# Kernel optimization log

Hardware: AMD Instinct MI355X
Metric: run time of the kernel (lower is better)

Reference implementation:

```python
import jax, jax.numpy as jnp
import numpy as np

BETA = 0.25


def setup_inputs() -> dict:
    key = jax.random.key(0)
    k1, k2 = jax.random.split(key)
    N, K, D = 65536, 1024, 256
    z = jax.random.normal(k1, (N, D), dtype=jnp.float32)
    # EmbeddingEMA initializes weight uniform in [-1, 1]
    weight = jax.random.uniform(k2, (K, D), dtype=jnp.float32, minval=-1.0, maxval=1.0)
    return {"z": z, "weight": weight}


def reference(z, weight):
    # z: [N, D] flattened latents; weight: [K, D] codebook
    z_flat = z.reshape(-1, weight.shape[1])
    # squared euclidean distances via ||z||^2 + ||e||^2 - 2 z e^T
    d = (
        jnp.sum(z_flat * z_flat, axis=1, keepdims=True)
        + jnp.sum(weight * weight, axis=1)
        - 2.0 * jnp.matmul(z_flat, weight.T)
    )  # [N, K]
    min_encoding_indices = jnp.argmin(d, axis=1)  # [N]
    z_q = weight[min_encoding_indices].reshape(z.shape)  # embedding lookup
    # commitment loss: beta * mse(stop_grad(z_q), z)
    loss = BETA * jnp.mean((jax.lax.stop_gradient(z_q) - z) ** 2)
    # straight-through estimator
    z_q_st = z + jax.lax.stop_gradient(z_q - z)
    return (loss, z_q_st, min_encoding_indices)
```

## Files before the change

### kernel.cpp

```cpp
#include <hip/hip_runtime.h>
#include <hip/hip_bf16.h>

typedef float f32x4 __attribute__((ext_vector_type(4)));
typedef short short8 __attribute__((ext_vector_type(8)));

#define NTOT   65536
#define DDIM   256
#define KCODES 1024
#define BRR    128
#define CT     64
#define IDXOFF 16777217
#define MARGIN_T4 0.015f


__device__ __forceinline__ unsigned short bf16_rne(float x) {
  unsigned u = __float_as_uint(x);
  return (unsigned short)((u + 0x7fff + ((u >> 16) & 1)) >> 16);
}

__global__ __launch_bounds__(256) void wsq_kernel(const float* __restrict__ w,
                                                  float* __restrict__ wsq) {
  int k = blockIdx.x * 256 + threadIdx.x;
  if (k >= KCODES) return;
  const f32x4* wr = (const f32x4*)(w + (size_t)k * DDIM);
  float s = 0.f;
#pragma unroll 8
  for (int j = 0; j < DDIM / 4; ++j) {
    f32x4 v = wr[j];
    s += v[0] * v[0] + v[1] * v[1] + v[2] * v[2] + v[3] * v[3];
  }
  wsq[k] = s;
}

__global__ __launch_bounds__(256) void prep_w(const float* __restrict__ w,
                                              float* __restrict__ wplanes) {
  int t = blockIdx.x * 256 + threadIdx.x;
  int k = t >> 6;
  int d = (t & 63) * 4;
  f32x4 v = *(const f32x4*)(w + (size_t)k * DDIM + d);
  unsigned h[4], l[4];
#pragma unroll
  for (int j = 0; j < 4; ++j) {
    unsigned short hb = bf16_rne(v[j]);
    float hf = __uint_as_float(((unsigned)hb) << 16);
    h[j] = hb;
    l[j] = bf16_rne(v[j] - hf);
  }
  int ct = k >> 6, row = k & 63, dc = d >> 6, dloc = d & 63;
  size_t base = (size_t)(ct * 4 + dc) * 16384;
  int off = row * 128 + ((dloc * 2) ^ ((row & 7) << 4));
  *(int2*)((char*)wplanes + base + off) =
      make_int2((int)(h[0] | (h[1] << 16)), (int)(h[2] | (h[3] << 16)));
  *(int2*)((char*)wplanes + base + 8192 + off) =
      make_int2((int)(l[0] | (l[1] << 16)), (int)(l[2] | (l[3] << 16)));
}

__device__ __forceinline__ void stage_tile_z(const float* __restrict__ gsrc,
                                             short* hi_t, short* lo_t, int tid) {
#pragma unroll
  for (int it = 0; it < 8; ++it) {
    int flat4 = it * 256 + tid;
    int row = flat4 >> 4;
    int c4 = (flat4 & 15) * 4;
    f32x4 v = *(const f32x4*)(gsrc + (size_t)row * DDIM + c4);
    unsigned h[4], l[4];
#pragma unroll
    for (int j = 0; j < 4; ++j) {
      unsigned short hb = bf16_rne(v[j]);
      float hf = __uint_as_float(((unsigned)hb) << 16);
      h[j] = hb;
      l[j] = bf16_rne(v[j] - hf);
    }
    int off = row * 128 + ((c4 * 2) ^ ((row & 7) << 4));
    *(int2*)((char*)hi_t + off) = make_int2((int)(h[0] | (h[1] << 16)), (int)(h[2] | (h[3] << 16)));
    *(int2*)((char*)lo_t + off) = make_int2((int)(l[0] | (l[1] << 16)), (int)(l[2] | (l[3] << 16)));
  }
}

__device__ __forceinline__ void stage_w2(const float* __restrict__ wpl, int pr,
                                         char* buf, int tid) {
  const char* g = (const char*)wpl + (size_t)pr * 32768 + tid * 16;
  char* l = buf + ((tid >> 6) << 10);
#pragma unroll
  for (int i = 0; i < 8; ++i)
    __builtin_amdgcn_global_load_lds(
        (const __attribute__((address_space(1))) unsigned int*)(g + i * 4096),
        (__attribute__((address_space(3))) unsigned int*)(l + i * 4096), 16, 0, 0);
}

#define INS4(S0, S1, S2, S3, I0, I1, I2, I3, os, oi)                        \
  if (os < S3 || (os == S3 && oi < I3)) {                                   \
    if (os < S2 || (os == S2 && oi < I2)) {                                 \
      S3 = S2; I3 = I2;                                                     \
      if (os < S1 || (os == S1 && oi < I1)) {                               \
        S2 = S1; I2 = I1;                                                   \
        if (os < S0 || (os == S0 && oi < I0)) {                             \
          S1 = S0; I1 = I0; S0 = os; I0 = oi;                               \
        } else { S1 = os; I1 = oi; }                                        \
      } else { S2 = os; I2 = oi; }                                          \
    } else { S3 = os; I3 = oi; }                                            \
  }

#define MFMA_STEP(DC, TB)                                                   \
  {                                                                         \
    _Pragma("unroll")                                                       \
    for (int ks = 0; ks < 2; ++ks) {                                        \
      _Pragma("unroll")                                                     \
      for (int mi = 0; mi < 4; ++mi) {                                      \
        const int row = mi * 16 + l15;                                      \
        const int off = row * 128 + (((ks * 64) + (lg * 16)) ^ ((row & 7) << 4)); \
        short8 ah = *(const short8*)((TB) + off);                           \
        short8 al = *(const short8*)((TB) + 8192 + off);                    \
        acc[mi][0] = __builtin_amdgcn_mfma_f32_16x16x32_bf16(ah, zf[DC][ks][0][0], acc[mi][0], 0, 0, 0); \
        acc[mi][0] = __builtin_amdgcn_mfma_f32_16x16x32_bf16(ah, zf[DC][ks][0][1], acc[mi][0], 0, 0, 0); \
        acc[mi][0] = __builtin_amdgcn_mfma_f32_16x16x32_bf16(al, zf[DC][ks][0][0], acc[mi][0], 0, 0, 0); \
        acc[mi][1] = __builtin_amdgcn_mfma_f32_16x16x32_bf16(ah, zf[DC][ks][1][0], acc[mi][1], 0, 0, 0); \
        acc[mi][1] = __builtin_amdgcn_mfma_f32_16x16x32_bf16(ah, zf[DC][ks][1][1], acc[mi][1], 0, 0, 0); \
        acc[mi][1] = __builtin_amdgcn_mfma_f32_16x16x32_bf16(al, zf[DC][ks][1][0], acc[mi][1], 0, 0, 0); \
      }                                                                     \
    }                                                                       \
  }

__global__ __launch_bounds__(256, 2) void vq_main(
    const float* __restrict__ z, const float* __restrict__ wplanes,
    const float* __restrict__ wsq, int* __restrict__ cand,
    int* __restrict__ flags, int* __restrict__ cnt, int* __restrict__ list) {
  __shared__ __align__(16) char lds[69632];
  char* buf0 = lds;
  char* buf1 = lds + 32768;
  float* wsq_l = (float*)(lds + 65536);

  const int tid = threadIdx.x;
  const int lane = tid & 63, wid = tid >> 6;
  const int l15 = lane & 15, lg = lane >> 4;
  const int br = blockIdx.x * BRR;

  for (int i = tid; i < KCODES; i += 256) wsq_l[i] = wsq[i];

  short8 zf[4][2][2][2];
  {
    short* zhi = (short*)lds;
    short* zlo = (short*)(lds + 16384);
    const int row0 = wid * 32 + l15, row1 = row0 + 16;
#pragma unroll
    for (int dc = 0; dc < 4; ++dc) {
      __syncthreads();
      stage_tile_z(z + (size_t)br * DDIM + dc * 64, zhi, zlo, tid);
      __syncthreads();
#pragma unroll
      for (int ks = 0; ks < 2; ++ks) {
        const int kb2 = (ks * 32 + lg * 8) * 2;
        const int off0 = row0 * 128 + (kb2 ^ ((row0 & 7) << 4));
        const int off1 = row1 * 128 + (kb2 ^ ((row1 & 7) << 4));
        zf[dc][ks][0][0] = *(const short8*)((char*)zhi + off0);
        zf[dc][ks][0][1] = *(const short8*)((char*)zlo + off0);
        zf[dc][ks][1][0] = *(const short8*)((char*)zhi + off1);
        zf[dc][ks][1][1] = *(const short8*)((char*)zlo + off1);
      }
    }
    __syncthreads();
  }

  float a0 = 3.4e38f, a1 = 3.4e38f, a2 = 3.4e38f, a3 = 3.4e38f;
  int e0 = 0x7fffffff, e1 = 0x7fffffff, e2 = 0x7fffffff, e3 = 0x7fffffff;
  float c0 = 3.4e38f, c1 = 3.4e38f, c2 = 3.4e38f, c3 = 3.4e38f;
  int f0 = 0x7fffffff, f1 = 0x7fffffff, f2 = 0x7fffffff, f3 = 0x7fffffff;

  stage_w2(wplanes, 0, buf0, tid);
  __syncthreads();

  for (int ct = 0; ct < 16; ++ct) {
    f32x4 acc[4][2];
#pragma unroll
    for (int mi = 0; mi < 4; ++mi)
#pragma unroll
      for (int ni = 0; ni < 2; ++ni) acc[mi][ni] = (f32x4){0.f, 0.f, 0.f, 0.f};

    stage_w2(wplanes, ct * 2 + 1, buf1, tid);
    MFMA_STEP(0, buf0)
    MFMA_STEP(1, buf0 + 16384)
    __syncthreads();
    if (ct < 15) stage_w2(wplanes, ct * 2 + 2, buf0, tid);
    MFMA_STEP(2, buf1)
    MFMA_STEP(3, buf1 + 16384)
    __syncthreads();

    const int kb = ct * CT;
#pragma unroll
    for (int mi = 0; mi < 4; ++mi)
#pragma unroll
      for (int rg = 0; rg < 4; ++rg) {
        const int cg = kb + mi * 16 + lg * 4 + rg;
        const float w2 = wsq_l[cg];
        float s0v = fmaf(-2.f, acc[mi][0][rg], w2);
        if (s0v < a3 || (s0v == a3 && cg < e3)) { INS4(a0, a1, a2, a3, e0, e1, e2, e3, s0v, cg); }
        float s1v = fmaf(-2.f, acc[mi][1][rg], w2);
        if (s1v < c3 || (s1v == c3 && cg < f3)) { INS4(c0, c1, c2, c3, f0, f1, f2, f3, s1v, cg); }
      }
  }

#pragma unroll
  for (int m = 16; m <= 32; m <<= 1) {
    float os[4]; int oi[4];
    os[0] = __shfl_xor(a0, m); oi[0] = __shfl_xor(e0, m);
    os[1] = __shfl_xor(a1, m); oi[1] = __shfl_xor(e1, m);
    os[2] = __shfl_xor(a2, m); oi[2] = __shfl_xor(e2, m);
    os[3] = __shfl_xor(a3, m); oi[3] = __shfl_xor(e3, m);
#pragma unroll
    for (int t = 0; t < 4; ++t) { INS4(a0, a1, a2, a3, e0, e1, e2, e3, os[t], oi[t]); }
    os[0] = __shfl_xor(c0, m); oi[0] = __shfl_xor(f0, m);
    os[1] = __shfl_xor(c1, m); oi[1] = __shfl_xor(f1, m);
    os[2] = __shfl_xor(c2, m); oi[2] = __shfl_xor(f2, m);
    os[3] = __shfl_xor(c3, m); oi[3] = __shfl_xor(f3, m);
#pragma unroll
    for (int t = 0; t < 4; ++t) { INS4(c0, c1, c2, c3, f0, f1, f2, f3, os[t], oi[t]); }
  }

  if (lg == 0) {
    {
      int grow = br + wid * 32 + l15;
      *(int4*)&cand[(size_t)grow * 4] = make_int4(e0, e1, e2, e3);
      int flg = (a3 - a0 < MARGIN_T4) ? 1 : 0;
      flags[grow] = flg;
      if (flg) { int p = atomicAdd(cnt, 1); list[p] = grow; }
    }
    {
      int grow = br + wid * 32 + 16 + l15;
      *(int4*)&cand[(size_t)grow * 4] = make_int4(f0, f1, f2, f3);
      int flg = (c3 - c0 < MARGIN_T4) ? 1 : 0;
      flags[grow] = flg;
      if (flg) { int p = atomicAdd(cnt, 1); list[p] = grow; }
    }
  }
}

__global__ __launch_bounds__(256) void refine_fused(
    const float* __restrict__ z, const float* __restrict__ w,
    const float* __restrict__ wsq, const int* __restrict__ cand,
    const int* __restrict__ flags, float* __restrict__ buckets,
    float* __restrict__ out) {
  __shared__ float ws4[4];
  const int tid = threadIdx.x, lane = tid & 63, wv = tid >> 6;
  float lsum = 0.f;
  for (int r = blockIdx.x * 4 + wv; r < NTOT; r += gridDim.x * 4) {
    if (flags[r]) continue;
    const int4 c4 = *(const int4*)&cand[(size_t)r * 4];
    f32x4 zv = *(const f32x4*)(z + (size_t)r * DDIM + lane * 4);
    f32x4 w0 = *(const f32x4*)(w + (size_t)c4.x * DDIM + lane * 4);
    f32x4 w1 = *(const f32x4*)(w + (size_t)c4.y * DDIM + lane * 4);
    f32x4 w2 = *(const f32x4*)(w + (size_t)c4.z * DDIM + lane * 4);
    f32x4 w3 = *(const f32x4*)(w + (size_t)c4.w * DDIM + lane * 4);
    float p0 = fmaf(zv[0], w0[0], fmaf(zv[1], w0[1], fmaf(zv[2], w0[2], zv[3] * w0[3])));
    float p1 = fmaf(zv[0], w1[0], fmaf(zv[1], w1[1], fmaf(zv[2], w1[2], zv[3] * w1[3])));
    float p2 = fmaf(zv[0], w2[0], fmaf(zv[1], w2[1], fmaf(zv[2], w2[2], zv[3] * w2[3])));
    float p3 = fmaf(zv[0], w3[0], fmaf(zv[1], w3[1], fmaf(zv[2], w3[2], zv[3] * w3[3])));
#pragma unroll
    for (int m = 1; m <= 32; m <<= 1) {
      p0 += __shfl_xor(p0, m);
      p1 += __shfl_xor(p1, m);
      p2 += __shfl_xor(p2, m);
      p3 += __shfl_xor(p3, m);
    }
    float s0 = fmaf(-2.f, p0, wsq[c4.x]);
    float s1 = fmaf(-2.f, p1, wsq[c4.y]);
    float s2 = fmaf(-2.f, p2, wsq[c4.z]);
    float s3 = fmaf(-2.f, p3, wsq[c4.w]);
    float bs = s0; int bi = c4.x;
    if (s1 < bs || (s1 == bs && c4.y < bi)) { bs = s1; bi = c4.y; }
    if (s2 < bs || (s2 == bs && c4.z < bi)) { bs = s2; bi = c4.z; }
    if (s3 < bs || (s3 == bs && c4.w < bi)) { bs = s3; bi = c4.w; }
    f32x4 qv = *(const f32x4*)(w + (size_t)bi * DDIM + lane * 4);
    f32x4 o;
#pragma unroll
    for (int j = 0; j < 4; ++j) {
      float df = qv[j] - zv[j];
      o[j] = zv[j] + df;
      lsum = fmaf(df, df, lsum);
    }
    *(f32x4*)(out + 1 + (size_t)r * DDIM + lane * 4) = o;
    if (lane == 0) out[(size_t)IDXOFF + r] = (float)bi;
  }
#pragma unroll
  for (int m = 1; m <= 32; m <<= 1) lsum += __shfl_xor(lsum, m);
  if (lane == 0) ws4[wv] = lsum;
  __syncthreads();
  if (tid == 0)
    atomicAdd(&buckets[blockIdx.x & 63], ws4[0] + ws4[1] + ws4[2] + ws4[3]);
}

__global__ __launch_bounds__(256) void vq_refine(
    const float* __restrict__ z, const float* __restrict__ w,
    const float* __restrict__ wsq, float* __restrict__ buckets,
    const int* __restrict__ cnt, const int* __restrict__ list,
    float* __restrict__ out) {
  __shared__ __align__(16) float zrow[DDIM];
  __shared__ float rv[256];
  __shared__ int ri[256];
  const int tid = threadIdx.x;
  const int n = *cnt;
  for (int li = blockIdx.x; li < n; li += gridDim.x) {
    const int row = list[li];
    __syncthreads();
    zrow[tid] = z[(size_t)row * DDIM + tid];
    __syncthreads();
    float bv = 3.4e38f; int bi = 0;
#pragma unroll
    for (int c0 = 0; c0 < 4; ++c0) {
      int c = tid * 4 + c0;
      const f32x4* wr4 = (const f32x4*)(w + (size_t)c * DDIM);
      const f32x4* zr4 = (const f32x4*)zrow;
      f32x4 dv = {0.f, 0.f, 0.f, 0.f};
      for (int q = 0; q < DDIM / 4; ++q) {
        f32x4 a = zr4[q], b = wr4[q];
        dv[0] = fmaf(a[0], b[0], dv[0]); dv[1] = fmaf(a[1], b[1], dv[1]);
        dv[2] = fmaf(a[2], b[2], dv[2]); dv[3] = fmaf(a[3], b[3], dv[3]);
      }
      float s = fmaf(-2.f, (dv[0] + dv[1]) + (dv[2] + dv[3]), wsq[c]);
      if (s < bv) { bv = s; bi = c; }
    }
    rv[tid] = bv; ri[tid] = bi;
    __syncthreads();
    for (int s = 128; s > 0; s >>= 1) {
      if (tid < s) {
        float v2 = rv[tid + s]; int i2 = ri[tid + s];
        if (v2 < rv[tid] || (v2 == rv[tid] && i2 < ri[tid])) { rv[tid] = v2; ri[tid] = i2; }
      }
      __syncthreads();
    }
    const int idx = ri[0];
    if (tid == 0) out[(size_t)IDXOFF + row] = (float)idx;
    float qv = w[(size_t)idx * DDIM + tid];
    float zv = zrow[tid];
    float df = qv - zv;
    out[1 + (size_t)row * DDIM + tid] = zv + df;
    __syncthreads();
    rv[tid] = df * df;
    __syncthreads();
    for (int s = 128; s > 0; s >>= 1) {
      if (tid < s) rv[tid] += rv[tid + s];
      __syncthreads();
    }
    if (tid == 0) atomicAdd(&buckets[0], rv[0]);
  }
}

__global__ void vq_finalize(const float* __restrict__ buckets,
                            float* __restrict__ out) {
  float s = 0.f;
  for (int i = 0; i < 64; ++i) s += buckets[i];
  out[0] = 0.25f * s * (1.0f / 16777216.0f);
}

extern "C" void kernel_launch(void* const* d_in, const int* in_sizes, int n_in,
                              void* d_out, int out_size, void* d_ws, size_t ws_size,
                              hipStream_t stream) {
  const float* z = (const float*)d_in[0];
  const float* w = (const float*)d_in[1];
  float* out = (float*)d_out;
  float* wsf = (float*)d_ws;
  float* buckets = wsf;
  int* cnt = (int*)wsf + 64;
  float* wsq = wsf + 80;
  float* wplanes = wsf + 2048;
  int* cand = (int*)(wsf + 264192);
  int* flags = (int*)(wsf + 526336);
  int* list = (int*)(wsf + 591872);

  hipMemsetAsync(d_ws, 0, 320, stream);
  wsq_kernel<<<dim3(KCODES / 256), dim3(256), 0, stream>>>(w, wsq);
  prep_w<<<dim3(256), dim3(256), 0, stream>>>(w, wplanes);
  vq_main<<<dim3(NTOT / BRR), dim3(256), 0, stream>>>(z, wplanes, wsq, cand, flags, cnt, list);
  refine_fused<<<dim3(4096), dim3(256), 0, stream>>>(z, w, wsq, cand, flags, buckets, out);
  vq_refine<<<dim3(128), dim3(256), 0, stream>>>(z, w, wsq, buckets, cnt, list, out);
  vq_finalize<<<dim3(1), dim3(1), 0, stream>>>(buckets, out);
}
```

Measured before the change: 309.3 us.

## Fuse gather and loss into main VQ kernel, track top-2 with margin patch

Replaces the per-row top-4 candidate list and the separate candidate rescoring kernel with a top-2 margin check inside the main kernel. The main kernel now writes indices, gathers z_q, writes the output and accumulates the loss directly, so the cand/flags buffers and one launch disappear. Rows with a small top-2 gap are queued to a patch kernel that recomputes them exactly in fp32 and corrects the loss by a delta. The weight staging is split into smaller single-plane double-buffered chunks, which halves LDS use. The cost is more syncs per tile and a wider margin (0.04), which may queue more rows for the exact fp32 fallback.

```diff
diff --git a/kernel.cpp b/kernel.cpp
--- a/kernel.cpp
+++ b/kernel.cpp
@@ -10,7 +10,7 @@
 #define BRR    128
 #define CT     64
 #define IDXOFF 16777217
-#define MARGIN_T4 0.015f
+#define MARGIN 0.04f
 
 
 __device__ __forceinline__ unsigned short bf16_rne(float x) {
@@ -77,29 +77,16 @@
   }
 }
 
-__device__ __forceinline__ void stage_w2(const float* __restrict__ wpl, int pr,
-                                         char* buf, int tid) {
-  const char* g = (const char*)wpl + (size_t)pr * 32768 + tid * 16;
+__device__ __forceinline__ void stage_w(const float* __restrict__ wpl, int st,
+                                        char* buf, int tid) {
+  const char* g = (const char*)wpl + (size_t)st * 16384 + tid * 16;
   char* l = buf + ((tid >> 6) << 10);
 #pragma unroll
-  for (int i = 0; i < 8; ++i)
+  for (int i = 0; i < 4; ++i)
     __builtin_amdgcn_global_load_lds(
         (const __attribute__((address_space(1))) unsigned int*)(g + i * 4096),
         (__attribute__((address_space(3))) unsigned int*)(l + i * 4096), 16, 0, 0);
 }
-
-#define INS4(S0, S1, S2, S3, I0, I1, I2, I3, os, oi)                        \
-  if (os < S3 || (os == S3 && oi < I3)) {                                   \
-    if (os < S2 || (os == S2 && oi < I2)) {                                 \
-      S3 = S2; I3 = I2;                                                     \
-      if (os < S1 || (os == S1 && oi < I1)) {                               \
-        S2 = S1; I2 = I1;                                                   \
-        if (os < S0 || (os == S0 && oi < I0)) {                             \
-          S1 = S0; I1 = I0; S0 = os; I0 = oi;                               \
-        } else { S1 = os; I1 = oi; }                                        \
-      } else { S2 = os; I2 = oi; }                                          \
-    } else { S3 = os; I3 = oi; }                                            \
-  }
 
 #define MFMA_STEP(DC, TB)                                                   \
   {                                                                         \
@@ -122,13 +109,16 @@
   }
 
 __global__ __launch_bounds__(256, 2) void vq_main(
-    const float* __restrict__ z, const float* __restrict__ wplanes,
-    const float* __restrict__ wsq, int* __restrict__ cand,
-    int* __restrict__ flags, int* __restrict__ cnt, int* __restrict__ list) {
-  __shared__ __align__(16) char lds[69632];
+    const float* __restrict__ z, const float* __restrict__ w,
+    const float* __restrict__ wplanes, const float* __restrict__ wsq,
+    float* __restrict__ buckets, int* __restrict__ cnt, int* __restrict__ list,
+    float* __restrict__ out) {
+  __shared__ __align__(16) char lds[36864];
   char* buf0 = lds;
-  char* buf1 = lds + 32768;
-  float* wsq_l = (float*)(lds + 65536);
+  char* buf1 = lds + 16384;
+  float* wsq_l = (float*)(lds + 32768);
+  __shared__ int sidx[BRR];
+  __shared__ float ws4[4];
 
   const int tid = threadIdx.x;
   const int lane = tid & 63, wid = tid >> 6;
@@ -161,12 +151,10 @@
     __syncthreads();
   }
 
-  float a0 = 3.4e38f, a1 = 3.4e38f, a2 = 3.4e38f, a3 = 3.4e38f;
-  int e0 = 0x7fffffff, e1 = 0x7fffffff, e2 = 0x7fffffff, e3 = 0x7fffffff;
-  float c0 = 3.4e38f, c1 = 3.4e38f, c2 = 3.4e38f, c3 = 3.4e38f;
-  int f0 = 0x7fffffff, f1 = 0x7fffffff, f2 = 0x7fffffff, f3 = 0x7fffffff;
-
-  stage_w2(wplanes, 0, buf0, tid);
+  float m1[2] = {3.4e38f, 3.4e38f}, m2[2] = {3.4e38f, 3.4e38f};
+  int i1[2] = {0x7fffffff, 0x7fffffff};
+
+  stage_w(wplanes, 0, buf0, tid);
   __syncthreads();
 
   for (int ct = 0; ct < 16; ++ct) {
@@ -176,119 +164,75 @@
 #pragma unroll
       for (int ni = 0; ni < 2; ++ni) acc[mi][ni] = (f32x4){0.f, 0.f, 0.f, 0.f};
 
-    stage_w2(wplanes, ct * 2 + 1, buf1, tid);
-    MFMA_STEP(0, buf0)
-    MFMA_STEP(1, buf0 + 16384)
-    __syncthreads();
-    if (ct < 15) stage_w2(wplanes, ct * 2 + 2, buf0, tid);
-    MFMA_STEP(2, buf1)
-    MFMA_STEP(3, buf1 + 16384)
-    __syncthreads();
+#pragma unroll
+    for (int dc = 0; dc < 4; ++dc) {
+      const int st = ct * 4 + dc;
+      char* cbuf = (st & 1) ? buf1 : buf0;
+      char* nbuf = (st & 1) ? buf0 : buf1;
+      if (st < 63) stage_w(wplanes, st + 1, nbuf, tid);
+      MFMA_STEP(dc, cbuf)
+      __syncthreads();
+    }
 
     const int kb = ct * CT;
 #pragma unroll
-    for (int mi = 0; mi < 4; ++mi)
-#pragma unroll
-      for (int rg = 0; rg < 4; ++rg) {
-        const int cg = kb + mi * 16 + lg * 4 + rg;
-        const float w2 = wsq_l[cg];
-        float s0v = fmaf(-2.f, acc[mi][0][rg], w2);
-        if (s0v < a3 || (s0v == a3 && cg < e3)) { INS4(a0, a1, a2, a3, e0, e1, e2, e3, s0v, cg); }
-        float s1v = fmaf(-2.f, acc[mi][1][rg], w2);
-        if (s1v < c3 || (s1v == c3 && cg < f3)) { INS4(c0, c1, c2, c3, f0, f1, f2, f3, s1v, cg); }
+    for (int ni = 0; ni < 2; ++ni)
+#pragma unroll
+      for (int mi = 0; mi < 4; ++mi)
+#pragma unroll
+        for (int rg = 0; rg < 4; ++rg) {
+          const int cg = kb + mi * 16 + lg * 4 + rg;
+          float s = fmaf(-2.f, acc[mi][ni][rg], wsq_l[cg]);
+          if (s < m1[ni]) { m2[ni] = m1[ni]; m1[ni] = s; i1[ni] = cg; }
+          else if (s < m2[ni]) m2[ni] = s;
+        }
+  }
+
+#pragma unroll
+  for (int ni = 0; ni < 2; ++ni) {
+#pragma unroll
+    for (int m = 16; m <= 32; m <<= 1) {
+      float om1 = __shfl_xor(m1[ni], m);
+      float om2 = __shfl_xor(m2[ni], m);
+      int oi1 = __shfl_xor(i1[ni], m);
+      if (om1 < m1[ni] || (om1 == m1[ni] && oi1 < i1[ni])) {
+        m2[ni] = fminf(m1[ni], om2); m1[ni] = om1; i1[ni] = oi1;
+      } else {
+        m2[ni] = fminf(m2[ni], om1);
       }
-  }
-
-#pragma unroll
-  for (int m = 16; m <= 32; m <<= 1) {
-    float os[4]; int oi[4];
-    os[0] = __shfl_xor(a0, m); oi[0] = __shfl_xor(e0, m);
-    os[1] = __shfl_xor(a1, m); oi[1] = __shfl_xor(e1, m);
-    os[2] = __shfl_xor(a2, m); oi[2] = __shfl_xor(e2, m);
-    os[3] = __shfl_xor(a3, m); oi[3] = __shfl_xor(e3, m);
-#pragma unroll
-    for (int t = 0; t < 4; ++t) { INS4(a0, a1, a2, a3, e0, e1, e2, e3, os[t], oi[t]); }
-    os[0] = __shfl_xor(c0, m); oi[0] = __shfl_xor(f0, m);
-    os[1] = __shfl_xor(c1, m); oi[1] = __shfl_xor(f1, m);
-    os[2] = __shfl_xor(c2, m); oi[2] = __shfl_xor(f2, m);
-    os[3] = __shfl_xor(c3, m); oi[3] = __shfl_xor(f3, m);
-#pragma unroll
-    for (int t = 0; t < 4; ++t) { INS4(c0, c1, c2, c3, f0, f1, f2, f3, os[t], oi[t]); }
+    }
   }
 
   if (lg == 0) {
-    {
-      int grow = br + wid * 32 + l15;
-      *(int4*)&cand[(size_t)grow * 4] = make_int4(e0, e1, e2, e3);
-      int flg = (a3 - a0 < MARGIN_T4) ? 1 : 0;
-      flags[grow] = flg;
-      if (flg) { int p = atomicAdd(cnt, 1); list[p] = grow; }
-    }
-    {
-      int grow = br + wid * 32 + 16 + l15;
-      *(int4*)&cand[(size_t)grow * 4] = make_int4(f0, f1, f2, f3);
-      int flg = (c3 - c0 < MARGIN_T4) ? 1 : 0;
-      flags[grow] = flg;
-      if (flg) { int p = atomicAdd(cnt, 1); list[p] = grow; }
-    }
-  }
-}
-
-__global__ __launch_bounds__(256) void refine_fused(
-    const float* __restrict__ z, const float* __restrict__ w,
-    const float* __restrict__ wsq, const int* __restrict__ cand,
-    const int* __restrict__ flags, float* __restrict__ buckets,
-    float* __restrict__ out) {
-  __shared__ float ws4[4];
-  const int tid = threadIdx.x, lane = tid & 63, wv = tid >> 6;
+#pragma unroll
+    for (int ni = 0; ni < 2; ++ni) {
+      int rl = wid * 32 + ni * 16 + l15;
+      int grow = br + rl;
+      sidx[rl] = i1[ni];
+      out[(size_t)IDXOFF + grow] = (float)i1[ni];
+      if (m2[ni] - m1[ni] < MARGIN) { int p = atomicAdd(cnt, 1); list[p] = grow; }
+    }
+  }
+  __syncthreads();
+
   float lsum = 0.f;
-  for (int r = blockIdx.x * 4 + wv; r < NTOT; r += gridDim.x * 4) {
-    if (flags[r]) continue;
-    const int4 c4 = *(const int4*)&cand[(size_t)r * 4];
-    f32x4 zv = *(const f32x4*)(z + (size_t)r * DDIM + lane * 4);
-    f32x4 w0 = *(const f32x4*)(w + (size_t)c4.x * DDIM + lane * 4);
-    f32x4 w1 = *(const f32x4*)(w + (size_t)c4.y * DDIM + lane * 4);
-    f32x4 w2 = *(const f32x4*)(w + (size_t)c4.z * DDIM + lane * 4);
-    f32x4 w3 = *(const f32x4*)(w + (size_t)c4.w * DDIM + lane * 4);
-    float p0 = fmaf(zv[0], w0[0], fmaf(zv[1], w0[1], fmaf(zv[2], w0[2], zv[3] * w0[3])));
-    float p1 = fmaf(zv[0], w1[0], fmaf(zv[1], w1[1], fmaf(zv[2], w1[2], zv[3] * w1[3])));
-    float p2 = fmaf(zv[0], w2[0], fmaf(zv[1], w2[1], fmaf(zv[2], w2[2], zv[3] * w2[3])));
-    float p3 = fmaf(zv[0], w3[0], fmaf(zv[1], w3[1], fmaf(zv[2], w3[2], zv[3] * w3[3])));
-#pragma unroll
-    for (int m = 1; m <= 32; m <<= 1) {
-      p0 += __shfl_xor(p0, m);
-      p1 += __shfl_xor(p1, m);
-      p2 += __shfl_xor(p2, m);
-      p3 += __shfl_xor(p3, m);
-    }
-    float s0 = fmaf(-2.f, p0, wsq[c4.x]);
-    float s1 = fmaf(-2.f, p1, wsq[c4.y]);
-    float s2 = fmaf(-2.f, p2, wsq[c4.z]);
-    float s3 = fmaf(-2.f, p3, wsq[c4.w]);
-    float bs = s0; int bi = c4.x;
-    if (s1 < bs || (s1 == bs && c4.y < bi)) { bs = s1; bi = c4.y; }
-    if (s2 < bs || (s2 == bs && c4.z < bi)) { bs = s2; bi = c4.z; }
-    if (s3 < bs || (s3 == bs && c4.w < bi)) { bs = s3; bi = c4.w; }
-    f32x4 qv = *(const f32x4*)(w + (size_t)bi * DDIM + lane * 4);
-    f32x4 o;
-#pragma unroll
-    for (int j = 0; j < 4; ++j) {
-      float df = qv[j] - zv[j];
-      o[j] = zv[j] + df;
-      lsum = fmaf(df, df, lsum);
-    }
-    *(f32x4*)(out + 1 + (size_t)r * DDIM + lane * 4) = o;
-    if (lane == 0) out[(size_t)IDXOFF + r] = (float)bi;
-  }
-#pragma unroll
-  for (int m = 1; m <= 32; m <<= 1) lsum += __shfl_xor(lsum, m);
-  if (lane == 0) ws4[wv] = lsum;
+  for (int r = 0; r < BRR; ++r) {
+    int idx = sidx[r];
+    float qv = w[(size_t)idx * DDIM + tid];
+    float zv = z[(size_t)(br + r) * DDIM + tid];
+    float df = qv - zv;
+    out[1 + (size_t)(br + r) * DDIM + tid] = zv + df;
+    lsum = fmaf(df, df, lsum);
+  }
+#pragma unroll
+  for (int m = 32; m > 0; m >>= 1) lsum += __shfl_down(lsum, m, 64);
+  if (lane == 0) ws4[wid] = lsum;
   __syncthreads();
   if (tid == 0)
     atomicAdd(&buckets[blockIdx.x & 63], ws4[0] + ws4[1] + ws4[2] + ws4[3]);
 }
 
-__global__ __launch_bounds__(256) void vq_refine(
+__global__ __launch_bounds__(256) void patch(
     const float* __restrict__ z, const float* __restrict__ w,
     const float* __restrict__ wsq, float* __restrict__ buckets,
     const int* __restrict__ cnt, const int* __restrict__ list,
@@ -328,19 +272,20 @@
       __syncthreads();
     }
     const int idx = ri[0];
+    const int old = (int)out[(size_t)IDXOFF + row];
     if (tid == 0) out[(size_t)IDXOFF + row] = (float)idx;
-    float qv = w[(size_t)idx * DDIM + tid];
     float zv = zrow[tid];
-    float df = qv - zv;
-    out[1 + (size_t)row * DDIM + tid] = zv + df;
-    __syncthreads();
-    rv[tid] = df * df;
+    float dfn = w[(size_t)idx * DDIM + tid] - zv;
+    float dfo = w[(size_t)old * DDIM + tid] - zv;
+    out[1 + (size_t)row * DDIM + tid] = zv + dfn;
+    __syncthreads();
+    rv[tid] = dfn * dfn - dfo * dfo;
     __syncthreads();
     for (int s = 128; s > 0; s >>= 1) {
       if (tid < s) rv[tid] += rv[tid + s];
       __syncthreads();
     }
-    if (tid == 0) atomicAdd(&buckets[0], rv[0]);
+    if (tid == 0) atomicAdd(&buckets[row & 63], rv[0]);
   }
 }
 
@@ -362,15 +307,12 @@
   int* cnt = (int*)wsf + 64;
   float* wsq = wsf + 80;
   float* wplanes = wsf + 2048;
-  int* cand = (int*)(wsf + 264192);
-  int* flags = (int*)(wsf + 526336);
-  int* list = (int*)(wsf + 591872);
+  int* list = (int*)(wsf + 264192);
 
   hipMemsetAsync(d_ws, 0, 320, stream);
   wsq_kernel<<<dim3(KCODES / 256), dim3(256), 0, stream>>>(w, wsq);
   prep_w<<<dim3(256), dim3(256), 0, stream>>>(w, wplanes);
-  vq_main<<<dim3(NTOT / BRR), dim3(256), 0, stream>>>(z, wplanes, wsq, cand, flags, cnt, list);
-  refine_fused<<<dim3(4096), dim3(256), 0, stream>>>(z, w, wsq, cand, flags, buckets, out);
-  vq_refine<<<dim3(128), dim3(256), 0, stream>>>(z, w, wsq, buckets, cnt, list, out);
+  vq_main<<<dim3(NTOT / BRR), dim3(256), 0, stream>>>(z, w, wplanes, wsq, buckets, cnt, list, out);
+  patch<<<dim3(1024), dim3(256), 0, stream>>>(z, w, wsq, buckets, cnt, list, out);
   vq_finalize<<<dim3(1), dim3(1), 0, stream>>>(buckets, out);
 }
```

Result: slower. 683.7 us (+121.1%).

## Fuse gather/loss epilogue into main kernel and patch only ambiguous rows

Applied to the files above, without the earlier changes.

The main distance kernel now writes the provisional argmin index, the straight-through output and the loss contribution itself. The separate pass that re-read every row is replaced by a patch kernel that only handles rows whose top-1/top-2 gap is under a margin. Those rows re-score the 4 candidates in fp32 and correct the output and loss by a delta. Rows whose 4th candidate is also within the margin go to a full-scan kernel. W staging is also split into smaller 16KB chunks, which halves the LDS footprint and may allow more blocks per CU. The risks are a row-serial epilogue loop inside the main kernel and a wider margin (0.05) that routes more rows to patching.

```diff
diff --git a/kernel.cpp b/kernel.cpp
--- a/kernel.cpp
+++ b/kernel.cpp
@@ -10,7 +10,7 @@
 #define BRR    128
 #define CT     64
 #define IDXOFF 16777217
-#define MARGIN_T4 0.015f
+#define MARGIN 0.05f
 
 
 __device__ __forceinline__ unsigned short bf16_rne(float x) {
@@ -77,12 +77,12 @@
   }
 }
 
-__device__ __forceinline__ void stage_w2(const float* __restrict__ wpl, int pr,
-                                         char* buf, int tid) {
-  const char* g = (const char*)wpl + (size_t)pr * 32768 + tid * 16;
+__device__ __forceinline__ void stage_w(const float* __restrict__ wpl, int st,
+                                        char* buf, int tid) {
+  const char* g = (const char*)wpl + (size_t)st * 16384 + tid * 16;
   char* l = buf + ((tid >> 6) << 10);
 #pragma unroll
-  for (int i = 0; i < 8; ++i)
+  for (int i = 0; i < 4; ++i)
     __builtin_amdgcn_global_load_lds(
         (const __attribute__((address_space(1))) unsigned int*)(g + i * 4096),
         (__attribute__((address_space(3))) unsigned int*)(l + i * 4096), 16, 0, 0);
@@ -122,13 +122,17 @@
   }
 
 __global__ __launch_bounds__(256, 2) void vq_main(
-    const float* __restrict__ z, const float* __restrict__ wplanes,
-    const float* __restrict__ wsq, int* __restrict__ cand,
-    int* __restrict__ flags, int* __restrict__ cnt, int* __restrict__ list) {
-  __shared__ __align__(16) char lds[69632];
+    const float* __restrict__ z, const float* __restrict__ w,
+    const float* __restrict__ wplanes, const float* __restrict__ wsq,
+    float* __restrict__ buckets, int* __restrict__ cnt, int* __restrict__ cnt2,
+    int* __restrict__ list, int* __restrict__ list2, int* __restrict__ cand,
+    float* __restrict__ out) {
+  __shared__ __align__(16) char lds[36864];
   char* buf0 = lds;
-  char* buf1 = lds + 32768;
-  float* wsq_l = (float*)(lds + 65536);
+  char* buf1 = lds + 16384;
+  float* wsq_l = (float*)(lds + 32768);
+  __shared__ int sidx[BRR];
+  __shared__ float ws4[4];
 
   const int tid = threadIdx.x;
   const int lane = tid & 63, wid = tid >> 6;
@@ -166,7 +170,7 @@
   float c0 = 3.4e38f, c1 = 3.4e38f, c2 = 3.4e38f, c3 = 3.4e38f;
   int f0 = 0x7fffffff, f1 = 0x7fffffff, f2 = 0x7fffffff, f3 = 0x7fffffff;
 
-  stage_w2(wplanes, 0, buf0, tid);
+  stage_w(wplanes, 0, buf0, tid);
   __syncthreads();
 
   for (int ct = 0; ct < 16; ++ct) {
@@ -176,14 +180,15 @@
 #pragma unroll
       for (int ni = 0; ni < 2; ++ni) acc[mi][ni] = (f32x4){0.f, 0.f, 0.f, 0.f};
 
-    stage_w2(wplanes, ct * 2 + 1, buf1, tid);
-    MFMA_STEP(0, buf0)
-    MFMA_STEP(1, buf0 + 16384)
-    __syncthreads();
-    if (ct < 15) stage_w2(wplanes, ct * 2 + 2, buf0, tid);
-    MFMA_STEP(2, buf1)
-    MFMA_STEP(3, buf1 + 16384)
-    __syncthreads();
+#pragma unroll
+    for (int dc = 0; dc < 4; ++dc) {
+      const int st = ct * 4 + dc;
+      char* cbuf = (st & 1) ? buf1 : buf0;
+      char* nbuf = (st & 1) ? buf0 : buf1;
+      if (st < 63) stage_w(wplanes, st + 1, nbuf, tid);
+      MFMA_STEP(dc, cbuf)
+      __syncthreads();
+    }
 
     const int kb = ct * CT;
 #pragma unroll
@@ -218,33 +223,61 @@
 
   if (lg == 0) {
     {
-      int grow = br + wid * 32 + l15;
-      *(int4*)&cand[(size_t)grow * 4] = make_int4(e0, e1, e2, e3);
-      int flg = (a3 - a0 < MARGIN_T4) ? 1 : 0;
-      flags[grow] = flg;
-      if (flg) { int p = atomicAdd(cnt, 1); list[p] = grow; }
+      int rl = wid * 32 + l15;
+      int grow = br + rl;
+      sidx[rl] = e0;
+      out[(size_t)IDXOFF + grow] = (float)e0;
+      if (a1 - a0 < MARGIN) {
+        bool needfull = (a3 - a0 < MARGIN);
+        *(int4*)&cand[(size_t)grow * 4] = make_int4(needfull ? -1 : e0, e1, e2, e3);
+        int p = atomicAdd(cnt, 1); list[p] = grow;
+        if (needfull) { int q = atomicAdd(cnt2, 1); list2[q] = grow; }
+      }
     }
     {
-      int grow = br + wid * 32 + 16 + l15;
-      *(int4*)&cand[(size_t)grow * 4] = make_int4(f0, f1, f2, f3);
-      int flg = (c3 - c0 < MARGIN_T4) ? 1 : 0;
-      flags[grow] = flg;
-      if (flg) { int p = atomicAdd(cnt, 1); list[p] = grow; }
-    }
-  }
-}
-
-__global__ __launch_bounds__(256) void refine_fused(
+      int rl = wid * 32 + 16 + l15;
+      int grow = br + rl;
+      sidx[rl] = f0;
+      out[(size_t)IDXOFF + grow] = (float)f0;
+      if (c1 - c0 < MARGIN) {
+        bool needfull = (c3 - c0 < MARGIN);
+        *(int4*)&cand[(size_t)grow * 4] = make_int4(needfull ? -1 : f0, f1, f2, f3);
+        int p = atomicAdd(cnt, 1); list[p] = grow;
+        if (needfull) { int q = atomicAdd(cnt2, 1); list2[q] = grow; }
+      }
+    }
+  }
+  __syncthreads();
+
+  float lsum = 0.f;
+  for (int r = 0; r < BRR; ++r) {
+    int idx = sidx[r];
+    float qv = w[(size_t)idx * DDIM + tid];
+    float zv = z[(size_t)(br + r) * DDIM + tid];
+    float df = qv - zv;
+    out[1 + (size_t)(br + r) * DDIM + tid] = zv + df;
+    lsum = fmaf(df, df, lsum);
+  }
+#pragma unroll
+  for (int m = 32; m > 0; m >>= 1) lsum += __shfl_down(lsum, m, 64);
+  if (lane == 0) ws4[wid] = lsum;
+  __syncthreads();
+  if (tid == 0)
+    atomicAdd(&buckets[blockIdx.x & 63], ws4[0] + ws4[1] + ws4[2] + ws4[3]);
+}
+
+__global__ __launch_bounds__(256) void patch_lite(
     const float* __restrict__ z, const float* __restrict__ w,
-    const float* __restrict__ wsq, const int* __restrict__ cand,
-    const int* __restrict__ flags, float* __restrict__ buckets,
-    float* __restrict__ out) {
-  __shared__ float ws4[4];
+    const float* __restrict__ wsq, const int* __restrict__ cnt,
+    const int* __restrict__ list, const int* __restrict__ cand,
+    float* __restrict__ buckets, float* __restrict__ out) {
   const int tid = threadIdx.x, lane = tid & 63, wv = tid >> 6;
-  float lsum = 0.f;
-  for (int r = blockIdx.x * 4 + wv; r < NTOT; r += gridDim.x * 4) {
-    if (flags[r]) continue;
+  const int n = *cnt;
+  float dloss = 0.f;
+  for (int li = blockIdx.x * 4 + wv; li < n; li += gridDim.x * 4) {
+    const int r = list[li];
     const int4 c4 = *(const int4*)&cand[(size_t)r * 4];
+    if (c4.x < 0) continue;
     f32x4 zv = *(const f32x4*)(z + (size_t)r * DDIM + lane * 4);
     f32x4 w0 = *(const f32x4*)(w + (size_t)c4.x * DDIM + lane * 4);
     f32x4 w1 = *(const f32x4*)(w + (size_t)c4.y * DDIM + lane * 4);
@@ -269,37 +302,39 @@
     if (s1 < bs || (s1 == bs && c4.y < bi)) { bs = s1; bi = c4.y; }
     if (s2 < bs || (s2 == bs && c4.z < bi)) { bs = s2; bi = c4.z; }
     if (s3 < bs || (s3 == bs && c4.w < bi)) { bs = s3; bi = c4.w; }
-    f32x4 qv = *(const f32x4*)(w + (size_t)bi * DDIM + lane * 4);
-    f32x4 o;
-#pragma unroll
-    for (int j = 0; j < 4; ++j) {
-      float df = qv[j] - zv[j];
-      o[j] = zv[j] + df;
-      lsum = fmaf(df, df, lsum);
-    }
-    *(f32x4*)(out + 1 + (size_t)r * DDIM + lane * 4) = o;
-    if (lane == 0) out[(size_t)IDXOFF + r] = (float)bi;
-  }
-#pragma unroll
-  for (int m = 1; m <= 32; m <<= 1) lsum += __shfl_xor(lsum, m);
-  if (lane == 0) ws4[wv] = lsum;
-  __syncthreads();
-  if (tid == 0)
-    atomicAdd(&buckets[blockIdx.x & 63], ws4[0] + ws4[1] + ws4[2] + ws4[3]);
-}
-
-__global__ __launch_bounds__(256) void vq_refine(
+    if (bi != c4.x) {
+      f32x4 qn = *(const f32x4*)(w + (size_t)bi * DDIM + lane * 4);
+      f32x4 o;
+      float d2 = 0.f;
+#pragma unroll
+      for (int j = 0; j < 4; ++j) {
+        float dfn = qn[j] - zv[j];
+        float dfo = w0[j] - zv[j];
+        o[j] = zv[j] + dfn;
+        d2 += dfn * dfn - dfo * dfo;
+      }
+      *(f32x4*)(out + 1 + (size_t)r * DDIM + lane * 4) = o;
+      if (lane == 0) out[(size_t)IDXOFF + r] = (float)bi;
+      dloss += d2;
+    }
+  }
+#pragma unroll
+  for (int m = 1; m <= 32; m <<= 1) dloss += __shfl_xor(dloss, m);
+  if (lane == 0 && dloss != 0.f) atomicAdd(&buckets[blockIdx.x & 63], dloss);
+}
+
+__global__ __launch_bounds__(256) void full_scan(
     const float* __restrict__ z, const float* __restrict__ w,
     const float* __restrict__ wsq, float* __restrict__ buckets,
-    const int* __restrict__ cnt, const int* __restrict__ list,
+    const int* __restrict__ cnt2, const int* __restrict__ list2,
     float* __restrict__ out) {
   __shared__ __align__(16) float zrow[DDIM];
   __shared__ float rv[256];
   __shared__ int ri[256];
   const int tid = threadIdx.x;
-  const int n = *cnt;
+  const int n = *cnt2;
   for (int li = blockIdx.x; li < n; li += gridDim.x) {
-    const int row = list[li];
+    const int row = list2[li];
     __syncthreads();
     zrow[tid] = z[(size_t)row * DDIM + tid];
     __syncthreads();
@@ -328,19 +363,20 @@
       __syncthreads();
     }
     const int idx = ri[0];
+    const int old = (int)out[(size_t)IDXOFF + row];
     if (tid == 0) out[(size_t)IDXOFF + row] = (float)idx;
-    float qv = w[(size_t)idx * DDIM + tid];
     float zv = zrow[tid];
-    float df = qv - zv;
-    out[1 + (size_t)row * DDIM + tid] = zv + df;
-    __syncthreads();
-    rv[tid] = df * df;
+    float dfn = w[(size_t)idx * DDIM + tid] - zv;
+    float dfo = w[(size_t)old * DDIM + tid] - zv;
+    out[1 + (size_t)row * DDIM + tid] = zv + dfn;
+    __syncthreads();
+    rv[tid] = dfn * dfn - dfo * dfo;
     __syncthreads();
     for (int s = 128; s > 0; s >>= 1) {
       if (tid < s) rv[tid] += rv[tid + s];
       __syncthreads();
     }
-    if (tid == 0) atomicAdd(&buckets[0], rv[0]);
+    if (tid == 0) atomicAdd(&buckets[row & 63], rv[0]);
   }
 }
 
@@ -360,17 +396,19 @@
   float* wsf = (float*)d_ws;
   float* buckets = wsf;
   int* cnt = (int*)wsf + 64;
+  int* cnt2 = (int*)wsf + 65;
   float* wsq = wsf + 80;
   float* wplanes = wsf + 2048;
   int* cand = (int*)(wsf + 264192);
-  int* flags = (int*)(wsf + 526336);
-  int* list = (int*)(wsf + 591872);
+  int* list = (int*)(wsf + 526336);
+  int* list2 = (int*)(wsf + 591872);
 
   hipMemsetAsync(d_ws, 0, 320, stream);
   wsq_kernel<<<dim3(KCODES / 256), dim3(256), 0, stream>>>(w, wsq);
   prep_w<<<dim3(256), dim3(256), 0, stream>>>(w, wplanes);
-  vq_main<<<dim3(NTOT / BRR), dim3(256), 0, stream>>>(z, wplanes, wsq, cand, flags, cnt, list);
-  refine_fused<<<dim3(4096), dim3(256), 0, stream>>>(z, w, wsq, cand, flags, buckets, out);
-  vq_refine<<<dim3(128), dim3(256), 0, stream>>>(z, w, wsq, buckets, cnt, list, out);
+  vq_main<<<dim3(NTOT / BRR), dim3(256), 0, stream>>>(z, w, wplanes, wsq, buckets,
+                                                      cnt, cnt2, list, list2, cand, out);
+  patch_lite<<<dim3(2048), dim3(256), 0, stream>>>(z, w, wsq, cnt, list, cand, buckets, out);
+  full_scan<<<dim3(1024), dim3(256), 0, stream>>>(z, w, wsq, buckets, cnt2, list2, out);
   vq_finalize<<<dim3(1), dim3(1), 0, stream>>>(buckets, out);
 }
```

After: 289.8 us. -6.3%, faster.
